# Kernel tuning notes

Hardware: AMD Instinct MI355X
Metric: run time of the kernel (lower is better)

The kernel has to match this reference:

```python
import jax, jax.numpy as jnp
import numpy as np

LAYER_SIZES = [1024, 1024, 1024, 1024, 1024, 1024, 512]
MAX_PATHS = 128
BATCH = 128
N_LAYERS = len(LAYER_SIZES) - 1


def setup_inputs() -> dict:
    key = jax.random.key(0)
    keys = jax.random.split(key, 1 + 2 * N_LAYERS)
    inp = {"x": jax.random.normal(keys[0], (BATCH, LAYER_SIZES[0]), dtype=jnp.float32)}
    for i in range(N_LAYERS):
        inp[f"W{i}"] = jax.random.normal(keys[1 + 2 * i], (LAYER_SIZES[i], LAYER_SIZES[i + 1]), dtype=jnp.float32) * 0.01
        inp[f"b{i}"] = jax.random.normal(keys[2 + 2 * i], (LAYER_SIZES[i + 1],), dtype=jnp.float32) * 0.01
    return inp


def _layer(data, W, b):
    # data: [B, in_feat, P] -> [B, out_feat, 3P]
    B, _, P = data.shape
    O = W.shape[1]
    pos = jnp.einsum('bfp,fo->bpo', data, W) + b          # [B, P, O]; neg branch is exactly -pos
    branches = jnp.stack([-pos, jnp.zeros_like(pos), pos], axis=-1)  # [B, P, O, 3]
    # transpose(1,2) then reshape: interleave branches per source path, matching torch
    return branches.transpose(0, 2, 1, 3).reshape(B, O, P * 3)


def _prune(data, keep):
    # keep top-`keep` paths by L2 norm over the feature dim
    norms = jnp.linalg.norm(data, axis=1)                 # [B, P]
    _, idx = jax.lax.top_k(norms, keep)                   # [B, keep]
    return jnp.take_along_axis(data, idx[:, None, :], axis=-1)


def _forward(x, Ws, bs):
    data = x[:, :, None]                                   # [B, F, 1]
    for i in range(N_LAYERS):
        data = _layer(data, Ws[i], bs[i])
        if i < N_LAYERS - 1:
            data = jnp.tanh(data)
        if data.shape[-1] > MAX_PATHS:
            data = _prune(data, MAX_PATHS)
    # collapse with 'max_abs': per (batch, feature) pick path with largest |value|
    idx = jnp.argmax(jnp.abs(data), axis=-1, keepdims=True)
    output = jnp.take_along_axis(data, idx, axis=-1).squeeze(-1)
    return output, data


def reference(x, W0, b0, W1, b1, W2, b2, W3, b3, W4, b4, W5, b5):
    Ws = [W0, W1, W2, W3, W4, W5]
    bs = [b0, b1, b2, b3, b4, b5]
    return _forward(x, Ws, bs)
```

## Files before the change

### kernel.cpp

```cpp
#include <hip/hip_runtime.h>
#include <math.h>


using s8v = __attribute__((ext_vector_type(8))) short;
using f4v = __attribute__((ext_vector_type(4))) float;

__device__ __forceinline__ float bf2f(short b) {
  unsigned u = ((unsigned)(unsigned short)b) << 16;
  return __builtin_bit_cast(float, u);
}
__device__ __forceinline__ short f2bf(float f) {
  unsigned u = __builtin_bit_cast(unsigned, f);
  u = (u + 0x7FFFu + ((u >> 16) & 1u)) >> 16;
  return (short)u;
}
__device__ __forceinline__ void split_store(float f, short* hi, short* lo) {
  short h = f2bf(f);
  *hi = h;
  *lo = f2bf(f - bf2f(h));
}

struct TWArgs {
  const float* W[6];
  short* Th[6];
  short* Tl[6];
};
__global__ void __launch_bounds__(256)
transW_all(TWArgs a, const float* __restrict__ x, short* __restrict__ A0h,
           short* __restrict__ A0l) {
  __shared__ float tile[64][65];
  const int t = threadIdx.x;
  if (blockIdx.z == 6) {
    const int bf = blockIdx.y * 16 + blockIdx.x;
    if (bf < 128) {
      int i = (bf * 256 + t) * 4;
      float4 v = *(const float4*)&x[i];
      short4 h, l;
      h.x = f2bf(v.x); l.x = f2bf(v.x - bf2f(h.x));
      h.y = f2bf(v.y); l.y = f2bf(v.y - bf2f(h.y));
      h.z = f2bf(v.z); l.z = f2bf(v.z - bf2f(h.z));
      h.w = f2bf(v.w); l.w = f2bf(v.w - bf2f(h.w));
      *(short4*)&A0h[i] = h;
      *(short4*)&A0l[i] = l;
    }
    return;
  }
  const int z = blockIdx.z;
  const int N = (z == 5) ? 512 : 1024;
  const int n0 = blockIdx.x * 64, k0 = blockIdx.y * 64;
  if (n0 >= N) return;
  const float* __restrict__ W = a.W[z];
  short* __restrict__ Th = a.Th[z];
  short* __restrict__ Tl = a.Tl[z];
  const int r = t >> 4, c4 = (t & 15) * 4;
#pragma unroll
  for (int i = 0; i < 4; ++i) {
    int rr = r + 16 * i;
    float4 v = *(const float4*)&W[(size_t)(k0 + rr) * N + n0 + c4];
    tile[rr][c4 + 0] = v.x;
    tile[rr][c4 + 1] = v.y;
    tile[rr][c4 + 2] = v.z;
    tile[rr][c4 + 3] = v.w;
  }
  __syncthreads();
#pragma unroll
  for (int i = 0; i < 4; ++i) {
    int n = r + 16 * i;
    short4 h, l;
    float f0 = tile[c4 + 0][n], f1 = tile[c4 + 1][n];
    float f2 = tile[c4 + 2][n], f3 = tile[c4 + 3][n];
    h.x = f2bf(f0); l.x = f2bf(f0 - bf2f(h.x));
    h.y = f2bf(f1); l.y = f2bf(f1 - bf2f(h.y));
    h.z = f2bf(f2); l.z = f2bf(f2 - bf2f(h.z));
    h.w = f2bf(f3); l.w = f2bf(f3 - bf2f(h.w));
    size_t o = (size_t)(n0 + n) * 1024 + k0 + c4;
    *(short4*)&Th[o] = h;
    *(short4*)&Tl[o] = l;
  }
}

template <int MODE, int D, int KS>
__device__ __forceinline__ void gemm_body(
    int bx, int by, int bz, int R, const short* __restrict__ Ah,
    const short* __restrict__ Al, const short* __restrict__ Bh,
    const short* __restrict__ Bl, const float* __restrict__ bias,
    short* __restrict__ Oh, short* __restrict__ Ol, float* __restrict__ Of,
    int N, int Dn) {
  constexpr int KC = 1024 / KS;
  constexpr int BKP = 40;
  __shared__ short As_h[64 * BKP], As_l[64 * BKP];
  __shared__ short Bs_h[64 * BKP], Bs_l[64 * BKP];
  const int t = threadIdx.x;
  const int row0 = by * 64;
  const int col0 = bx * 64;
  const int kb = bz * KC;
  const int sr = t >> 2, sko = (t & 3) * 8;
  const short* Ahp = Ah + (size_t)(row0 + sr) * 1024 + kb + sko;
  const short* Alp = Al + (size_t)(row0 + sr) * 1024 + kb + sko;
  const short* Bhp = Bh + (size_t)(col0 + sr) * 1024 + kb + sko;
  const short* Blp = Bl + (size_t)(col0 + sr) * 1024 + kb + sko;
  const int w = t >> 6, lane = t & 63;
  const int l16 = lane & 15, q = lane >> 4;
  const int wm0 = (w & 1) * 32, wn0 = (w >> 1) * 32;
  const int abase = (wm0 + l16) * BKP + q * 8;
  const int bbase = (wn0 + l16) * BKP + q * 8;
  f4v acc[2][2];
#pragma unroll
  for (int i = 0; i < 2; ++i)
#pragma unroll
    for (int j = 0; j < 2; ++j) acc[i][j] = (f4v){0.f, 0.f, 0.f, 0.f};
  uint4 rah = *(const uint4*)(Ahp);
  uint4 ral = *(const uint4*)(Alp);
  uint4 rbh = *(const uint4*)(Bhp);
  uint4 rbl = *(const uint4*)(Blp);
  for (int k0 = 0; k0 < KC; k0 += 32) {
    __syncthreads();
    *(uint4*)&As_h[sr * BKP + sko] = rah;
    *(uint4*)&As_l[sr * BKP + sko] = ral;
    *(uint4*)&Bs_h[sr * BKP + sko] = rbh;
    *(uint4*)&Bs_l[sr * BKP + sko] = rbl;
    if (k0 + 32 < KC) {
      rah = *(const uint4*)(Ahp + k0 + 32);
      ral = *(const uint4*)(Alp + k0 + 32);
      rbh = *(const uint4*)(Bhp + k0 + 32);
      rbl = *(const uint4*)(Blp + k0 + 32);
    }
    __syncthreads();
    s8v ah[2], al[2], bh[2], bl[2];
#pragma unroll
    for (int mt = 0; mt < 2; ++mt) {
      ah[mt] = *(const s8v*)&As_h[abase + mt * 16 * BKP];
      al[mt] = *(const s8v*)&As_l[abase + mt * 16 * BKP];
    }
#pragma unroll
    for (int nt = 0; nt < 2; ++nt) {
      bh[nt] = *(const s8v*)&Bs_h[bbase + nt * 16 * BKP];
      bl[nt] = *(const s8v*)&Bs_l[bbase + nt * 16 * BKP];
    }
#pragma unroll
    for (int mt = 0; mt < 2; ++mt)
#pragma unroll
      for (int nt = 0; nt < 2; ++nt) {
        acc[mt][nt] = __builtin_amdgcn_mfma_f32_16x16x32_bf16(
            ah[mt], bh[nt], acc[mt][nt], 0, 0, 0);
        acc[mt][nt] = __builtin_amdgcn_mfma_f32_16x16x32_bf16(
            ah[mt], bl[nt], acc[mt][nt], 0, 0, 0);
        acc[mt][nt] = __builtin_amdgcn_mfma_f32_16x16x32_bf16(
            al[mt], bh[nt], acc[mt][nt], 0, 0, 0);
      }
  }
#pragma unroll
  for (int nt = 0; nt < 2; ++nt) {
    int gcol = col0 + wn0 + nt * 16 + l16;
    float bc = (MODE == 1) ? bias[gcol] : 0.f;
#pragma unroll
    for (int mt = 0; mt < 2; ++mt) {
#pragma unroll
      for (int r = 0; r < 4; ++r) {
        float v = acc[mt][nt][r];
        int rr = row0 + wm0 + mt * 16 + q * 4 + r;
        if (MODE == 1) {
          int b = rr / D, u = rr - b * D;
          size_t ob = (size_t)(b * Dn) * N + gcol;
          size_t om = ob + (size_t)(1 + 2 * u) * N;
          size_t op = ob + (size_t)(2 + 2 * u) * N;
          split_store(tanhf(bc - v), &Oh[om], &Ol[om]);
          split_store(tanhf(bc + v), &Oh[op], &Ol[op]);
          if (u == 0) split_store(tanhf(bc), &Oh[ob], &Ol[ob]);
        } else if (MODE == 2) {
          Of[(size_t)rr * N + gcol] = v;
        } else {
          Of[((size_t)bz * R + rr) * N + gcol] = v;
        }
      }
    }
  }
}

template <int MODE, int D, int KS>
__global__ void __launch_bounds__(256, 2)
mfma_gemm(const short* __restrict__ Ah, const short* __restrict__ Al,
          const short* __restrict__ Bh, const short* __restrict__ Bl,
          const float* __restrict__ bias, short* __restrict__ Oh,
          short* __restrict__ Ol, float* __restrict__ Of, int N, int Dn) {
  gemm_body<MODE, D, KS>(blockIdx.x, blockIdx.y, blockIdx.z,
                         (int)gridDim.y << 6, Ah, Al, Bh, Bl, bias, Oh, Ol,
                         Of, N, Dn);
}

__device__ __forceinline__ void rownorm_body(const short* __restrict__ hi,
                                             const short* __restrict__ lo,
                                             float* __restrict__ ns, int row) {
  int t = threadIdx.x;
  size_t base = (size_t)row * 1024 + t * 4;
  short4 h = *(const short4*)&hi[base];
  short4 l = *(const short4*)&lo[base];
  float v0 = bf2f(h.x) + bf2f(l.x);
  float v1 = bf2f(h.y) + bf2f(l.y);
  float v2 = bf2f(h.z) + bf2f(l.z);
  float v3 = bf2f(h.w) + bf2f(l.w);
  float s = v0 * v0 + v1 * v1 + v2 * v2 + v3 * v3;
  __shared__ float red[256];
  red[t] = s;
  __syncthreads();
  for (int off = 128; off; off >>= 1) {
    if (t < off) red[t] += red[t + off];
    __syncthreads();
  }
  if (t == 0) ns[row] = red[0];
}

__global__ void __launch_bounds__(256, 2)
gemm5_rownorm(const short* __restrict__ C5h, const short* __restrict__ C5l,
              const short* __restrict__ W5h, const short* __restrict__ W5l,
              float* __restrict__ Y5, float* __restrict__ ns) {
  const int bid = blockIdx.x;
  if (bid < 496) {
    gemm_body<2, 31, 1>(bid & 7, bid >> 3, 0, 0, C5h, C5l, W5h, W5l, nullptr,
                        nullptr, nullptr, Y5, 512, 0);
  } else {
    rownorm_body(C5h, C5l, ns, bid - 496);
  }
}

template <int KS>
__global__ void __launch_bounds__(256)
comb0_hl(const float* __restrict__ P, const float* __restrict__ bias,
         short* __restrict__ Oh, short* __restrict__ Ol, int R, int N) {
  int i = blockIdx.x * 256 + threadIdx.x;
  int n4 = N >> 2;
  int r = i / n4, c4 = (i - r * n4) * 4;
  float4 y = *(const float4*)&P[(size_t)r * N + c4];
  size_t stride = (size_t)R * N;
#pragma unroll
  for (int ks = 1; ks < KS; ++ks) {
    const float4 p = *(const float4*)&P[ks * stride + (size_t)r * N + c4];
    y.x += p.x; y.y += p.y; y.z += p.z; y.w += p.w;
  }
  float4 bc = *(const float4*)(bias + c4);
  float t0 = tanhf(bc.x + y.x), t1 = tanhf(bc.y + y.y);
  float t2 = tanhf(bc.z + y.z), t3 = tanhf(bc.w + y.w);
  short4 h, l;
  h.x = f2bf(t0); l.x = f2bf(t0 - bf2f(h.x));
  h.y = f2bf(t1); l.y = f2bf(t1 - bf2f(h.y));
  h.z = f2bf(t2); l.z = f2bf(t2 - bf2f(h.z));
  h.w = f2bf(t3); l.w = f2bf(t3 - bf2f(h.w));
  *(short4*)&Oh[(size_t)r * N + c4] = h;
  *(short4*)&Ol[(size_t)r * N + c4] = l;
}

template <int KS, int D>
__global__ void __launch_bounds__(256)
comb1_hl(const float* __restrict__ P, const float* __restrict__ bias,
         short* __restrict__ Oh, short* __restrict__ Ol, int R, int N,
         int Dn) {
  int i = blockIdx.x * 256 + threadIdx.x;
  int n4 = N >> 2;
  int r = i / n4, c4 = (i - r * n4) * 4;
  int b = r / D, u = r - b * D;
  float4 y = *(const float4*)&P[(size_t)r * N + c4];
  size_t stride = (size_t)R * N;
#pragma unroll
  for (int ks = 1; ks < KS; ++ks) {
    const float4 p = *(const float4*)&P[ks * stride + (size_t)r * N + c4];
    y.x += p.x; y.y += p.y; y.z += p.z; y.w += p.w;
  }
  float4 bc = *(const float4*)(bias + c4);
  size_t ob = (size_t)(b * Dn) * N + c4;
  size_t om = ob + (size_t)(1 + 2 * u) * N;
  size_t op = ob + (size_t)(2 + 2 * u) * N;
  {
    float t0 = tanhf(bc.x - y.x), t1 = tanhf(bc.y - y.y);
    float t2 = tanhf(bc.z - y.z), t3 = tanhf(bc.w - y.w);
    short4 h, l;
    h.x = f2bf(t0); l.x = f2bf(t0 - bf2f(h.x));
    h.y = f2bf(t1); l.y = f2bf(t1 - bf2f(h.y));
    h.z = f2bf(t2); l.z = f2bf(t2 - bf2f(h.z));
    h.w = f2bf(t3); l.w = f2bf(t3 - bf2f(h.w));
    *(short4*)&Oh[om] = h;
    *(short4*)&Ol[om] = l;
  }
  {
    float t0 = tanhf(bc.x + y.x), t1 = tanhf(bc.y + y.y);
    float t2 = tanhf(bc.z + y.z), t3 = tanhf(bc.w + y.w);
    short4 h, l;
    h.x = f2bf(t0); l.x = f2bf(t0 - bf2f(h.x));
    h.y = f2bf(t1); l.y = f2bf(t1 - bf2f(h.y));
    h.z = f2bf(t2); l.z = f2bf(t2 - bf2f(h.z));
    h.w = f2bf(t3); l.w = f2bf(t3 - bf2f(h.w));
    *(short4*)&Oh[op] = h;
    *(short4*)&Ol[op] = l;
  }
  if (u == 0) {
    float t0 = tanhf(bc.x), t1 = tanhf(bc.y);
    float t2 = tanhf(bc.z), t3 = tanhf(bc.w);
    short4 h, l;
    h.x = f2bf(t0); l.x = f2bf(t0 - bf2f(h.x));
    h.y = f2bf(t1); l.y = f2bf(t1 - bf2f(h.y));
    h.z = f2bf(t2); l.z = f2bf(t2 - bf2f(h.z));
    h.w = f2bf(t3); l.w = f2bf(t3 - bf2f(h.w));
    *(short4*)&Oh[ob] = h;
    *(short4*)&Ol[ob] = l;
  }
}

__global__ void __launch_bounds__(256)
stats5_k(const float* __restrict__ Y5, const float* __restrict__ b5,
         float* __restrict__ dotv, float* __restrict__ nrmv) {
  int row = blockIdx.x;
  int t = threadIdx.x;
  __shared__ float rd[256], rn[256];
  const float* y = Y5 + (size_t)row * 512;
  float d = 0.f, n2 = 0.f;
  for (int o = t; o < 512; o += 256) {
    float v = y[o];
    d = fmaf(b5[o], v, d);
    n2 = fmaf(v, v, n2);
  }
  rd[t] = d;
  rn[t] = n2;
  __syncthreads();
  for (int off = 128; off; off >>= 1) {
    if (t < off) {
      rd[t] += rd[t + off];
      rn[t] += rn[t + off];
    }
    __syncthreads();
  }
  if (t == 0) {
    dotv[row] = rd[0];
    nrmv[row] = rn[0];
  }
}

__global__ void __launch_bounds__(384)
finalize_k(const float* __restrict__ Y5, const float* __restrict__ b5,
           const float* __restrict__ ns, const float* __restrict__ dotv,
           const float* __restrict__ nrmv, float* __restrict__ out,
           float* __restrict__ dataout) {
  const int b = blockIdx.y;
  const int o0 = blockIdx.x * 64;
  __shared__ float nss[31];
  __shared__ float rb[256];
  __shared__ float keyA[243];
  __shared__ int cls[243];
  __shared__ int k4s[128];
  __shared__ float pns[128];
  __shared__ float keyB[384];
  __shared__ int k5s[128];
  __shared__ float Ys[31][65];
  __shared__ float bias_s[64];
  __shared__ float vt[64][130];
  __shared__ float ra[64][4];
  __shared__ float rv[64][4];
  const int t = threadIdx.x;
  for (int idx = t; idx < 31 * 64; idx += 384) {
    int c = idx >> 6, o = idx & 63;
    Ys[c][o] = Y5[((size_t)b * 31 + c) * 512 + o0 + o];
  }
  if (t < 64) bias_s[t] = b5[o0 + t];
  if (t < 31) nss[t] = ns[b * 31 + t];
  if (t < 256) {
    float a = b5[t], c = b5[t + 256];
    rb[t] = fmaf(a, a, 0.f);
    rb[t] = fmaf(c, c, rb[t]);
  }
  __syncthreads();
  for (int off = 128; off; off >>= 1) {
    if (t < off) rb[t] += rb[t + off];
    __syncthreads();
  }
  const float nb5 = rb[0];
  if (t < 243) {
    int j = t / 3, t4 = t - 3 * j;
    int d0 = j / 27, d1 = (j / 9) % 3, d2 = (j / 3) % 3, d3 = j % 3;
    int u = 0;
    u = (d0 == 1) ? 0 : (1 + 2 * u + (d0 == 2));
    u = (d1 == 1) ? 0 : (1 + 2 * u + (d1 == 2));
    u = (d2 == 1) ? 0 : (1 + 2 * u + (d2 == 2));
    u = (d3 == 1) ? 0 : (1 + 2 * u + (d3 == 2));
    cls[t] = u;
    keyA[t] = (t4 == 1) ? 0.f : nss[u];
  }
  __syncthreads();
  if (t < 243) {
    float k = keyA[t];
    int rank = 0;
    for (int e = 0; e < 243; ++e) {
      float ke = keyA[e];
      rank += (ke > k) || (ke == k && e < t);
    }
    if (rank < 128) {
      int t4 = t - 3 * (t / 3);
      k4s[rank] = (cls[t] << 1) | (t4 == 2 ? 1 : 0);
    }
  }
  __syncthreads();
  if (t < 128) {
    int k4 = k4s[t];
    int c = k4 >> 1;
    float s = (k4 & 1) ? 1.f : -1.f;
    pns[t] = nb5 + nrmv[b * 31 + c] + s * 2.f * dotv[b * 31 + c];
  }
  __syncthreads();
  {
    const int m = t / 3, tt = t - 3 * m;
    keyB[t] = (tt == 1) ? 0.f : pns[m];
    __syncthreads();
    float k = keyB[t];
    int rank = 0;
    for (int e = 0; e < 384; ++e) {
      float ke = keyB[e];
      rank += (ke > k) || (ke == k && e < t);
    }
    if (rank < 128) k5s[rank] = (m << 1) | (tt == 2 ? 1 : 0);
  }
  __syncthreads();
  if (t < 256) {
    const int rr = t & 127, oh = t >> 7;
    int k5 = k5s[rr];
    int m = k5 >> 1;
    float sig = (k5 & 1) ? 1.f : -1.f;
    int k4 = k4s[m];
    int cc = k4 >> 1;
    float s4 = (k4 & 1) ? 1.f : -1.f;
    float afac = sig * s4;
#pragma unroll
    for (int ol = 0; ol < 32; ++ol) {
      int o = oh * 32 + ol;
      float v = sig * bias_s[o] + afac * Ys[cc][o];
      dataout[((size_t)b * 512 + o0 + o) * 128 + rr] = v;
      vt[o][rr] = v;
    }
  }
  __syncthreads();
  if (t < 256) {
    int o = t >> 2, q = t & 3;
    float bestv = vt[o][q * 32];
    float besta = fabsf(bestv);
    for (int i = 1; i < 32; ++i) {
      float v = vt[o][q * 32 + i];
      float a = fabsf(v);
      if (a > besta) {
        besta = a;
        bestv = v;
      }
    }
    ra[o][q] = besta;
    rv[o][q] = bestv;
  }
  __syncthreads();
  if (t < 64) {
    float ba = ra[t][0], bv = rv[t][0];
#pragma unroll
    for (int qq = 1; qq < 4; ++qq) {
      if (ra[t][qq] > ba) {
        ba = ra[t][qq];
        bv = rv[t][qq];
      }
    }
    out[(size_t)b * 512 + o0 + t] = bv;
  }
}

extern "C" void kernel_launch(void* const* d_in, const int* in_sizes, int n_in,
                              void* d_out, int out_size, void* d_ws,
                              size_t ws_size, hipStream_t stream) {
  const float* x = (const float*)d_in[0];
  const float* Wt[6];
  const float* bs[6];
  for (int i = 0; i < 6; ++i) {
    Wt[i] = (const float*)d_in[1 + 2 * i];
    bs[i] = (const float*)d_in[2 + 2 * i];
  }
  char* base = (char*)d_ws;
  short* A0h = (short*)(base + 0);
  short* A0l = (short*)(base + 262144);
  short* Wh[6], *Wl[6];
  {
    size_t off = 524288;
    for (int i = 0; i < 6; ++i) {
      size_t sz = (i < 5) ? 2097152 : 1048576;
      Wh[i] = (short*)(base + off);
      Wl[i] = (short*)(base + off + sz);
      off += 2 * sz;
    }
  }
  short* C1h = (short*)(base + 23592960), *C1l = (short*)(base + 23855104);
  short* C2h = (short*)(base + 24117248), *C2l = (short*)(base + 24903680);
  short* C3h = (short*)(base + 25690112), *C3l = (short*)(base + 27525120);
  short* C4h = (short*)(base + 29360128), *C4l = (short*)(base + 33292288);
  short* C5h = (short*)(base + 524288);
  short* C5l = (short*)(base + 8912896);
  float* PA = (float*)(base + 29360128);
  float* PB = (float*)(base + 524288);
  float* Y5 = (float*)(base + 23592960);
  float* ns = (float*)(base + 37224448);
  float* dotv = (float*)(base + 37240320);
  float* nrmv = (float*)(base + 37256192);
  float* outp = (float*)d_out;
  float* dataout = outp + 128 * 512;

  dim3 blk(256);
  TWArgs twa;
  for (int i = 0; i < 6; ++i) {
    twa.W[i] = Wt[i];
    twa.Th[i] = Wh[i];
    twa.Tl[i] = Wl[i];
  }
  transW_all<<<dim3(16, 16, 7), blk, 0, stream>>>(twa, x, A0h, A0l);
  mfma_gemm<3, 1, 4><<<dim3(16, 2, 4), blk, 0, stream>>>(
      A0h, A0l, Wh[0], Wl[0], nullptr, nullptr, nullptr, PA, 1024, 0);
  comb0_hl<4><<<dim3(128), blk, 0, stream>>>(PA, bs[0], C1h, C1l, 128, 1024);
  mfma_gemm<3, 1, 4><<<dim3(16, 2, 4), blk, 0, stream>>>(
      C1h, C1l, Wh[1], Wl[1], nullptr, nullptr, nullptr, PA, 1024, 0);
  comb1_hl<4, 1><<<dim3(128), blk, 0, stream>>>(PA, bs[1], C2h, C2l, 128, 1024,
                                                3);
  mfma_gemm<3, 3, 4><<<dim3(16, 6, 4), blk, 0, stream>>>(
      C2h, C2l, Wh[2], Wl[2], nullptr, nullptr, nullptr, PA, 1024, 0);
  comb1_hl<4, 3><<<dim3(384), blk, 0, stream>>>(PA, bs[2], C3h, C3l, 384, 1024,
                                                7);
  mfma_gemm<3, 7, 2><<<dim3(16, 14, 2), blk, 0, stream>>>(
      C3h, C3l, Wh[3], Wl[3], nullptr, nullptr, nullptr, PB, 1024, 0);
  comb1_hl<2, 7><<<dim3(896), blk, 0, stream>>>(PB, bs[3], C4h, C4l, 896, 1024,
                                                15);
  mfma_gemm<1, 15, 1><<<dim3(16, 30), blk, 0, stream>>>(
      C4h, C4l, Wh[4], Wl[4], bs[4], C5h, C5l, nullptr, 1024, 31);
  gemm5_rownorm<<<dim3(496 + 3968), blk, 0, stream>>>(C5h, C5l, Wh[5], Wl[5],
                                                      Y5, ns);
  stats5_k<<<dim3(3968), blk, 0, stream>>>(Y5, bs[5], dotv, nrmv);
  finalize_k<<<dim3(8, 128), dim3(384), 0, stream>>>(Y5, bs[5], ns, dotv,
                                                     nrmv, outp, dataout);
}
```

Before: 264.2 us.

## Hoist per-batch path pruning out of finalize into separate kernel; raise split-K

The top-k path selection for layers 4 and 5 ran redundantly in each of the 8 output-tile blocks per batch row. It now runs once per batch in a new prune45_k kernel, which writes the kept path indices to workspace. The slimmer finalize kernel uses 256 threads and reads those indices. The first two GEMMs also move from split-K 4 to 8 for more parallelism. This costs one extra launch and more partial-sum traffic for the combine kernels.

```diff
diff --git a/kernel.cpp b/kernel.cpp
--- a/kernel.cpp
+++ b/kernel.cpp
@@ -334,12 +334,10 @@
 }
 
 __global__ void __launch_bounds__(384)
-finalize_k(const float* __restrict__ Y5, const float* __restrict__ b5,
-           const float* __restrict__ ns, const float* __restrict__ dotv,
-           const float* __restrict__ nrmv, float* __restrict__ out,
-           float* __restrict__ dataout) {
-  const int b = blockIdx.y;
-  const int o0 = blockIdx.x * 64;
+prune45_k(const float* __restrict__ ns, const float* __restrict__ dotv,
+          const float* __restrict__ nrmv, const float* __restrict__ b5,
+          int* __restrict__ kept4, int* __restrict__ kept5) {
+  const int b = blockIdx.x, t = threadIdx.x;
   __shared__ float nss[31];
   __shared__ float rb[256];
   __shared__ float keyA[243];
@@ -347,18 +345,6 @@
   __shared__ int k4s[128];
   __shared__ float pns[128];
   __shared__ float keyB[384];
-  __shared__ int k5s[128];
-  __shared__ float Ys[31][65];
-  __shared__ float bias_s[64];
-  __shared__ float vt[64][130];
-  __shared__ float ra[64][4];
-  __shared__ float rv[64][4];
-  const int t = threadIdx.x;
-  for (int idx = t; idx < 31 * 64; idx += 384) {
-    int c = idx >> 6, o = idx & 63;
-    Ys[c][o] = Y5[((size_t)b * 31 + c) * 512 + o0 + o];
-  }
-  if (t < 64) bias_s[t] = b5[o0 + t];
   if (t < 31) nss[t] = ns[b * 31 + t];
   if (t < 256) {
     float a = b5[t], c = b5[t + 256];
@@ -392,7 +378,9 @@
     }
     if (rank < 128) {
       int t4 = t - 3 * (t / 3);
-      k4s[rank] = (cls[t] << 1) | (t4 == 2 ? 1 : 0);
+      int kv = (cls[t] << 1) | (t4 == 2 ? 1 : 0);
+      k4s[rank] = kv;
+      kept4[b * 128 + rank] = kv;
     }
   }
   __syncthreads();
@@ -403,52 +391,65 @@
     pns[t] = nb5 + nrmv[b * 31 + c] + s * 2.f * dotv[b * 31 + c];
   }
   __syncthreads();
-  {
-    const int m = t / 3, tt = t - 3 * m;
-    keyB[t] = (tt == 1) ? 0.f : pns[m];
-    __syncthreads();
-    float k = keyB[t];
-    int rank = 0;
-    for (int e = 0; e < 384; ++e) {
-      float ke = keyB[e];
-      rank += (ke > k) || (ke == k && e < t);
-    }
-    if (rank < 128) k5s[rank] = (m << 1) | (tt == 2 ? 1 : 0);
-  }
-  __syncthreads();
-  if (t < 256) {
-    const int rr = t & 127, oh = t >> 7;
-    int k5 = k5s[rr];
-    int m = k5 >> 1;
-    float sig = (k5 & 1) ? 1.f : -1.f;
-    int k4 = k4s[m];
-    int cc = k4 >> 1;
-    float s4 = (k4 & 1) ? 1.f : -1.f;
-    float afac = sig * s4;
-#pragma unroll
-    for (int ol = 0; ol < 32; ++ol) {
-      int o = oh * 32 + ol;
-      float v = sig * bias_s[o] + afac * Ys[cc][o];
-      dataout[((size_t)b * 512 + o0 + o) * 128 + rr] = v;
-      vt[o][rr] = v;
-    }
-  }
-  __syncthreads();
-  if (t < 256) {
-    int o = t >> 2, q = t & 3;
-    float bestv = vt[o][q * 32];
-    float besta = fabsf(bestv);
-    for (int i = 1; i < 32; ++i) {
-      float v = vt[o][q * 32 + i];
-      float a = fabsf(v);
-      if (a > besta) {
-        besta = a;
-        bestv = v;
-      }
-    }
-    ra[o][q] = besta;
-    rv[o][q] = bestv;
-  }
+  const int m = t / 3, tt = t - 3 * m;
+  keyB[t] = (tt == 1) ? 0.f : pns[m];
+  __syncthreads();
+  float k = keyB[t];
+  int rank = 0;
+  for (int e = 0; e < 384; ++e) {
+    float ke = keyB[e];
+    rank += (ke > k) || (ke == k && e < t);
+  }
+  if (rank < 128) kept5[b * 128 + rank] = (m << 1) | (tt == 2 ? 1 : 0);
+}
+
+__global__ void __launch_bounds__(256)
+finalize_k(const float* __restrict__ Y5, const float* __restrict__ b5,
+           const int* __restrict__ kept4, const int* __restrict__ kept5,
+           float* __restrict__ out, float* __restrict__ dataout) {
+  const int b = blockIdx.y;
+  const int o0 = blockIdx.x * 64;
+  __shared__ float Ys[31][65];
+  __shared__ float bias_s[64];
+  __shared__ float vt[64][130];
+  __shared__ float ra[64][4];
+  __shared__ float rv[64][4];
+  const int t = threadIdx.x;
+  for (int idx = t; idx < 31 * 64; idx += 256) {
+    int c = idx >> 6, o = idx & 63;
+    Ys[c][o] = Y5[((size_t)b * 31 + c) * 512 + o0 + o];
+  }
+  if (t < 64) bias_s[t] = b5[o0 + t];
+  const int rr = t & 127, oh = t >> 7;
+  int k5 = kept5[b * 128 + rr];
+  int m = k5 >> 1;
+  float sig = (k5 & 1) ? 1.f : -1.f;
+  int k4 = kept4[b * 128 + m];
+  int cc = k4 >> 1;
+  float s4 = (k4 & 1) ? 1.f : -1.f;
+  float afac = sig * s4;
+  __syncthreads();
+#pragma unroll
+  for (int ol = 0; ol < 32; ++ol) {
+    int o = oh * 32 + ol;
+    float v = sig * bias_s[o] + afac * Ys[cc][o];
+    dataout[((size_t)b * 512 + o0 + o) * 128 + rr] = v;
+    vt[o][rr] = v;
+  }
+  __syncthreads();
+  int o = t >> 2, q = t & 3;
+  float bestv = vt[o][q * 32];
+  float besta = fabsf(bestv);
+  for (int i = 1; i < 32; ++i) {
+    float v = vt[o][q * 32 + i];
+    float a = fabsf(v);
+    if (a > besta) {
+      besta = a;
+      bestv = v;
+    }
+  }
+  ra[o][q] = besta;
+  rv[o][q] = bestv;
   __syncthreads();
   if (t < 64) {
     float ba = ra[t][0], bv = rv[t][0];
@@ -498,6 +499,8 @@
   float* ns = (float*)(base + 37224448);
   float* dotv = (float*)(base + 37240320);
   float* nrmv = (float*)(base + 37256192);
+  int* kept4 = (int*)(base + 37272068);
+  int* kept5 = (int*)(base + 37337604);
   float* outp = (float*)d_out;
   float* dataout = outp + 128 * 512;
 
@@ -509,12 +512,12 @@
     twa.Tl[i] = Wl[i];
   }
   transW_all<<<dim3(16, 16, 7), blk, 0, stream>>>(twa, x, A0h, A0l);
-  mfma_gemm<3, 1, 4><<<dim3(16, 2, 4), blk, 0, stream>>>(
+  mfma_gemm<3, 1, 8><<<dim3(16, 2, 8), blk, 0, stream>>>(
       A0h, A0l, Wh[0], Wl[0], nullptr, nullptr, nullptr, PA, 1024, 0);
-  comb0_hl<4><<<dim3(128), blk, 0, stream>>>(PA, bs[0], C1h, C1l, 128, 1024);
-  mfma_gemm<3, 1, 4><<<dim3(16, 2, 4), blk, 0, stream>>>(
+  comb0_hl<8><<<dim3(128), blk, 0, stream>>>(PA, bs[0], C1h, C1l, 128, 1024);
+  mfma_gemm<3, 1, 8><<<dim3(16, 2, 8), blk, 0, stream>>>(
       C1h, C1l, Wh[1], Wl[1], nullptr, nullptr, nullptr, PA, 1024, 0);
-  comb1_hl<4, 1><<<dim3(128), blk, 0, stream>>>(PA, bs[1], C2h, C2l, 128, 1024,
+  comb1_hl<8, 1><<<dim3(128), blk, 0, stream>>>(PA, bs[1], C2h, C2l, 128, 1024,
                                                 3);
   mfma_gemm<3, 3, 4><<<dim3(16, 6, 4), blk, 0, stream>>>(
       C2h, C2l, Wh[2], Wl[2], nullptr, nullptr, nullptr, PA, 1024, 0);
@@ -529,6 +532,8 @@
   gemm5_rownorm<<<dim3(496 + 3968), blk, 0, stream>>>(C5h, C5l, Wh[5], Wl[5],
                                                       Y5, ns);
   stats5_k<<<dim3(3968), blk, 0, stream>>>(Y5, bs[5], dotv, nrmv);
-  finalize_k<<<dim3(8, 128), dim3(384), 0, stream>>>(Y5, bs[5], ns, dotv,
-                                                     nrmv, outp, dataout);
-}
+  prune45_k<<<dim3(128), dim3(384), 0, stream>>>(ns, dotv, nrmv, bs[5], kept4,
+                                                 kept5);
+  finalize_k<<<dim3(8, 128), blk, 0, stream>>>(Y5, bs[5], kept4, kept5, outp,
+                                               dataout);
+}
```

Result: faster. 235.3 us (-11.0%).
